# Kernel optimization log

Measured on AMD Instinct MI355X. Metric: run time of the kernel, lower is better.

The kernel has to match this reference:

```python
import jax, jax.numpy as jnp
import numpy as np

B, N, C = 4, 1370, 1024
H, DH = 16, C // 16
N_ROPE = 1369  # patch tokens covered by RoPE (prefix=1 CLS token)


def _rotate_half(x):
    x1, x2 = jnp.split(x, 2, axis=-1)
    return jnp.concatenate([-x2, x1], axis=-1)


def _rope_apply(x, sin, cos):
    return x * cos + _rotate_half(x) * sin


def setup_inputs() -> dict:
    key = jax.random.key(0)
    ks = jax.random.split(key, 7)
    return {
        "x": jax.random.normal(ks[0], (B, N, C), dtype=jnp.float32),
        "sin": jax.random.normal(ks[1], (N_ROPE, DH), dtype=jnp.float32),
        "cos": jax.random.normal(ks[2], (N_ROPE, DH), dtype=jnp.float32),
        "w_qkv": jax.random.normal(ks[3], (C, 3 * C), dtype=jnp.float32) * (C ** -0.5),
        "b_qkv": jax.random.normal(ks[4], (3 * C,), dtype=jnp.float32) * 0.02,
        "w_proj": jax.random.normal(ks[5], (C, C), dtype=jnp.float32) * (C ** -0.5),
        "b_proj": jax.random.normal(ks[6], (C,), dtype=jnp.float32) * 0.02,
    }


def reference(x, sin, cos, w_qkv, b_qkv, w_proj, b_proj):
    b, n, c = x.shape
    # QKV projection -> [3, B, H, N, DH]
    qkv = (x @ w_qkv + b_qkv).reshape(b, n, 3, H, DH).transpose(2, 0, 3, 1, 4)
    q, k, v = qkv[0], qkv[1], qkv[2]
    # RoPE on the last N_ROPE tokens (prefix tokens, e.g. CLS, left untouched)
    prefix = n - sin.shape[-2]
    q = jnp.concatenate([q[:, :, :prefix, :], _rope_apply(q[:, :, prefix:, :], sin, cos)], axis=-2)
    k = jnp.concatenate([k[:, :, :prefix, :], _rope_apply(k[:, :, prefix:, :], sin, cos)], axis=-2)
    # Full attention
    scale = 1.0 / jnp.sqrt(jnp.asarray(DH, dtype=x.dtype))
    attn = jnp.einsum('bhqd,bhkd->bhqk', q, k) * scale
    attn = jax.nn.softmax(attn, axis=-1)
    out = jnp.einsum('bhqk,bhkd->bhqd', attn, v)
    out = out.transpose(0, 2, 1, 3).reshape(b, n, c)
    return out @ w_proj + b_proj
```

## Files before the change

### kernel.cpp

```cpp
#include <hip/hip_runtime.h>
#include <hip/hip_bf16.h>

#define B_ 4
#define N_ 1370
#define C_ 1024
#define H_ 16
#define DH_ 64
#define NR_ 1369
#define M_ (B_*N_)
#define VTS_ 1408
#define ALS 64
#define PLS 72

#define QSCALE 0.1803368801111f

typedef _Float16 f16x8  __attribute__((ext_vector_type(8)));
typedef __bf16   bf16x8 __attribute__((ext_vector_type(8)));
typedef float    f32x4  __attribute__((ext_vector_type(4)));

__device__ __forceinline__ f16x8 ld_frag_h(const unsigned short* p) {
    uint4 u = *(const uint4*)p;
    return __builtin_bit_cast(f16x8, u);
}
__device__ __forceinline__ bf16x8 ld_frag_b(const unsigned short* p) {
    uint4 u = *(const uint4*)p;
    return __builtin_bit_cast(bf16x8, u);
}
__device__ __forceinline__ unsigned short f2h(float f) {
    _Float16 h = (_Float16)f;
    return __builtin_bit_cast(unsigned short, h);
}
__device__ __forceinline__ unsigned short f2bf(float f) {
    __hip_bfloat16 h = __float2bfloat16(f);
    return __builtin_bit_cast(unsigned short, h);
}
__device__ __forceinline__ bf16x8 ones_bf() {
    uint4 u = make_uint4(0x3F803F80u, 0x3F803F80u, 0x3F803F80u, 0x3F803F80u);
    return __builtin_bit_cast(bf16x8, u);
}

__device__ __forceinline__ void load_lds16(const unsigned short* g, unsigned short* l) {
    __builtin_amdgcn_global_load_lds(
        (const __attribute__((address_space(1))) unsigned int*)g,
        (__attribute__((address_space(3))) unsigned int*)l,
        16, 0, 0);
}

#define XBLK 5480
#define WQBLK 768
#define WPBLK 256
__global__ __launch_bounds__(256)
void prep_k(const float* __restrict__ x, unsigned short* __restrict__ xo,
            const float* __restrict__ wq, unsigned short* __restrict__ wqt,
            const float* __restrict__ wp, unsigned short* __restrict__ wpt)
{
    __shared__ unsigned short Th[64][68];
    int bid = blockIdx.x;
    if (bid < XBLK) {
        const int i = bid * 256 + threadIdx.x;
        float4 v = ((const float4*)x)[i];
        ushort4 h;
        h.x = f2h(v.x); h.y = f2h(v.y); h.z = f2h(v.z); h.w = f2h(v.w);
        ((ushort4*)xo)[i] = h;
        return;
    }
    bid -= XBLK;
    const float* w; unsigned short* wt; int Ncol, nb;
    if (bid < WQBLK) { w = wq; wt = wqt; Ncol = 3072; nb = 48; }
    else { bid -= WQBLK; w = wp; wt = wpt; Ncol = 1024; nb = 16; }
    const int tid = threadIdx.x, tx = tid & 15, ty = tid >> 4;
    const int n0 = (bid % nb) * 64, k0 = (bid / nb) * 64;
    #pragma unroll
    for (int i = 0; i < 4; ++i) {
        const int k = ty + i * 16;
        float4 v = *(const float4*)&w[(size_t)(k0 + k) * Ncol + n0 + tx * 4];
        Th[k][tx*4+0] = f2h(v.x); Th[k][tx*4+1] = f2h(v.y);
        Th[k][tx*4+2] = f2h(v.z); Th[k][tx*4+3] = f2h(v.w);
    }
    __syncthreads();
    #pragma unroll
    for (int i = 0; i < 4; ++i) {
        const int n = ty + i * 16;
        ushort4 o;
        o.x = Th[tx*4+0][n]; o.y = Th[tx*4+1][n]; o.z = Th[tx*4+2][n]; o.w = Th[tx*4+3][n];
        *(ushort4*)&wt[(size_t)(n0 + n) * 1024 + k0 + tx * 4] = o;
    }
}

__global__ __launch_bounds__(256)
void transpose_v_k(const unsigned short* __restrict__ v, unsigned short* __restrict__ vt) {
    __shared__ unsigned short Th[64][68];
    const int tid = threadIdx.x, tx = tid & 15, ty = tid >> 4;
    const int bh = blockIdx.y, t0 = blockIdx.x * 64;
    const unsigned short* vp = v + (size_t)bh * N_ * DH_;
    unsigned short* vtp = vt + (size_t)bh * DH_ * VTS_;
    #pragma unroll
    for (int i = 0; i < 4; ++i) {
        const int tok = ty + i * 16;
        const int gtok = t0 + tok;
        ushort4 val;
        if (gtok < N_) val = *(const ushort4*)&vp[(size_t)gtok * DH_ + tx * 4];
        else { val.x = 0; val.y = 0; val.z = 0; val.w = 0; }
        Th[tok][tx*4+0] = val.x; Th[tok][tx*4+1] = val.y;
        Th[tok][tx*4+2] = val.z; Th[tok][tx*4+3] = val.w;
    }
    __syncthreads();
    #pragma unroll
    for (int i = 0; i < 4; ++i) {
        const int d = ty + i * 16;
        ushort4 o;
        o.x = Th[tx*4+0][d]; o.y = Th[tx*4+1][d]; o.z = Th[tx*4+2][d]; o.w = Th[tx*4+3][d];
        *(ushort4*)&vtp[(size_t)d * VTS_ + t0 + tx * 4] = o;
    }
}

__global__ __launch_bounds__(512, 4)
void gemm_qkv8(const unsigned short* __restrict__ A, const unsigned short* __restrict__ Bt,
               const float* __restrict__ bias,
               unsigned short* __restrict__ qb, unsigned short* __restrict__ kb,
               unsigned short* __restrict__ vb,
               const float* __restrict__ sinp, const float* __restrict__ cosp)
{
    __shared__ __align__(16) unsigned short A_s[2][192 * 64];
    __shared__ __align__(16) unsigned short B_s[2][128 * 64];

    const int tid = threadIdx.x;
    const int wave = tid >> 6, lane = tid & 63;
    const int quad = lane >> 4, l16 = lane & 15;

    const int id  = blockIdx.x;
    const int lid = (id & 7) * 87 + (id >> 3);
    const int mblk = lid / 24, nblk = lid - mblk * 24;
    const int m0 = mblk * 192, n0 = nblk * 128;

    const int mwave = (wave >> 1) * 48;
    const int nwave = (wave & 1) * 64;

    const int srow = lane >> 3;
    const int gseg = (lane & 7) ^ srow;

    f32x4 acc[3][4] = {};

    auto stage = [&](int kc, int buf) {
        const int kof = kc * 64;
        #pragma unroll
        for (int i = 0; i < 3; ++i) {
            const int rbase = wave * 24 + i * 8;
            int arow = m0 + rbase + srow;
            if (arow > M_ - 1) arow = M_ - 1;
            load_lds16(A + (size_t)arow * 1024 + kof + gseg * 8, &A_s[buf][rbase * 64]);
        }
        #pragma unroll
        for (int i = 0; i < 2; ++i) {
            const int rbase = wave * 16 + i * 8;
            const int brow = n0 + rbase + srow;
            load_lds16(Bt + (size_t)brow * 1024 + kof + gseg * 8, &B_s[buf][rbase * 64]);
        }
    };

    stage(0, 0);

    for (int kc = 0; kc < 16; ++kc) {
        const int cur = kc & 1;
        __syncthreads();
        if (kc + 1 < 16) stage(kc + 1, cur ^ 1);

        #pragma unroll
        for (int kh = 0; kh < 2; ++kh) {
            const int soff = (((kh * 4 + quad) ^ (l16 & 7)) << 3);
            f16x8 a[3], b[4];
            #pragma unroll
            for (int t = 0; t < 3; ++t)
                a[t] = ld_frag_h(&A_s[cur][(mwave + t * 16 + l16) * 64 + soff]);
            #pragma unroll
            for (int t = 0; t < 4; ++t)
                b[t] = ld_frag_h(&B_s[cur][(nwave + t * 16 + l16) * 64 + soff]);
            #pragma unroll
            for (int i = 0; i < 3; ++i)
                #pragma unroll
                for (int j = 0; j < 4; ++j)
                    acc[i][j] = __builtin_amdgcn_mfma_f32_16x16x32_f16(a[i], b[j], acc[i][j], 0, 0, 0);
        }
    }

    const int nbase = n0 + nwave;
    const int part = nbase >> 10;
    const int h = (nbase & 1023) >> 6;
    #pragma unroll
    for (int i = 0; i < 3; ++i) {
        #pragma unroll
        for (int r = 0; r < 4; ++r) {
            const int gm = m0 + mwave + i * 16 + quad * 4 + r;
            if (gm >= M_) continue;
            const int b = gm / N_;
            const int tok = gm - b * N_;

            float val[4];
            #pragma unroll
            for (int j = 0; j < 4; ++j)
                val[j] = acc[i][j][r] + bias[nbase + j * 16 + l16];

            if (part < 2 && tok >= 1) {
                const float* sp = sinp + (size_t)(tok - 1) * DH_;
                const float* cp = cosp + (size_t)(tok - 1) * DH_;
                const float s0 = sp[l16],      s1 = sp[16 + l16];
                const float s2 = sp[32 + l16], s3 = sp[48 + l16];
                const float c0 = cp[l16],      c1 = cp[16 + l16];
                const float c2 = cp[32 + l16], c3 = cp[48 + l16];
                const float n0v = fmaf(val[0], c0, -val[2] * s0);
                const float n1v = fmaf(val[1], c1, -val[3] * s1);
                const float n2v = fmaf(val[2], c2,  val[0] * s2);
                const float n3v = fmaf(val[3], c3,  val[1] * s3);
                val[0] = n0v; val[1] = n1v; val[2] = n2v; val[3] = n3v;
            }

            const int bh = b * H_ + h;
            #pragma unroll
            for (int j = 0; j < 4; ++j) {
                const int d = j * 16 + l16;
                if (part == 0)      qb[((size_t)bh * N_ + tok) * DH_ + d] = f2h(val[j] * QSCALE);
                else if (part == 1) kb[((size_t)bh * N_ + tok) * DH_ + d] = f2h(val[j]);
                else                vb[((size_t)bh * N_ + tok) * DH_ + d] = f2bf(val[j]);
            }
        }
    }
}

__global__ __launch_bounds__(256)
void gemm_proj2(const unsigned short* __restrict__ A, const unsigned short* __restrict__ Bt,
                const float* __restrict__ bias, float* __restrict__ out)
{
    __shared__ __align__(16) unsigned short A_s[2][64 * 64];
    __shared__ __align__(16) unsigned short B_s[2][128 * 64];

    const int tid = threadIdx.x;
    const int wave = tid >> 6, lane = tid & 63;
    const int quad = lane >> 4, l16 = lane & 15;
    const int m0 = blockIdx.y * 64, n0 = blockIdx.x * 128;
    const int mwave = (wave & 1) * 32, nwave = (wave >> 1) * 64;

    const int srow = lane >> 3;
    const int gseg = (lane & 7) ^ srow;

    f32x4 acc[2][4] = {};

    auto stage = [&](int kc, int buf) {
        const int kof = kc * 64;
        #pragma unroll
        for (int i = 0; i < 2; ++i) {
            const int rbase = wave * 16 + i * 8;
            int arow = m0 + rbase + srow;
            if (arow > M_ - 1) arow = M_ - 1;
            load_lds16(A + (size_t)arow * 1024 + kof + gseg * 8, &A_s[buf][rbase * 64]);
        }
        #pragma unroll
        for (int i = 0; i < 4; ++i) {
            const int rbase = wave * 32 + i * 8;
            const int brow = n0 + rbase + srow;
            load_lds16(Bt + (size_t)brow * 1024 + kof + gseg * 8, &B_s[buf][rbase * 64]);
        }
    };

    stage(0, 0);

    for (int kc = 0; kc < 16; ++kc) {
        const int cur = kc & 1;
        __syncthreads();
        if (kc + 1 < 16) stage(kc + 1, cur ^ 1);

        #pragma unroll
        for (int kh = 0; kh < 2; ++kh) {
            const int soff = (((kh * 4 + quad) ^ (l16 & 7)) << 3);
            f16x8 a[2], b[4];
            #pragma unroll
            for (int t = 0; t < 2; ++t)
                a[t] = ld_frag_h(&A_s[cur][(mwave + t * 16 + l16) * 64 + soff]);
            #pragma unroll
            for (int t = 0; t < 4; ++t)
                b[t] = ld_frag_h(&B_s[cur][(nwave + t * 16 + l16) * 64 + soff]);
            #pragma unroll
            for (int i = 0; i < 2; ++i)
                #pragma unroll
                for (int j = 0; j < 4; ++j)
                    acc[i][j] = __builtin_amdgcn_mfma_f32_16x16x32_f16(a[i], b[j], acc[i][j], 0, 0, 0);
        }
    }

    #pragma unroll
    for (int i = 0; i < 2; ++i) {
        #pragma unroll
        for (int r = 0; r < 4; ++r) {
            const int gm = m0 + mwave + i * 16 + quad * 4 + r;
            if (gm >= M_) continue;
            #pragma unroll
            for (int j = 0; j < 4; ++j) {
                const int gn = n0 + nwave + j * 16 + l16;
                out[(size_t)gm * 1024 + gn] = acc[i][j][r] + bias[gn];
            }
        }
    }
}

__global__ __launch_bounds__(512, 6)
void attn_k(const unsigned short* __restrict__ q, const unsigned short* __restrict__ k,
            const unsigned short* __restrict__ vt, unsigned short* __restrict__ out)
{
    __shared__ __align__(16) unsigned short Ks[2][64 * ALS];
    __shared__ __align__(16) unsigned short Vs[2][64 * ALS];
    __shared__ __align__(16) unsigned short Ps[8 * 16 * PLS];

    const int tid  = threadIdx.x;
    const int wave = tid >> 6, lane = tid & 63;
    const int quad = lane >> 4, l16 = lane & 15;
    const int srow = lane >> 3;
    const int gseg = (lane & 7) ^ srow;

    const int id  = blockIdx.x;
    const int lid = (id & 7) * 88 + (id >> 3);
    const int bh  = lid / 11;
    const int q0  = (lid - bh * 11) * 128;

    const unsigned short* qp  = q  + (size_t)bh * N_ * DH_;
    const unsigned short* kp  = k  + (size_t)bh * N_ * DH_;
    const unsigned short* vtp = vt + (size_t)bh * DH_ * VTS_;

    f16x8 qf[2];
    {
        int qrow = q0 + wave * 16 + l16;
        if (qrow > N_ - 1) qrow = N_ - 1;
        qf[0] = ld_frag_h(qp + (size_t)qrow * DH_ + quad * 8);
        qf[1] = ld_frag_h(qp + (size_t)qrow * DH_ + 32 + quad * 8);
    }

    const bf16x8 onesv = ones_bf();
    f32x4 O[4] = {};
    f32x4 L = {};

    unsigned short* Pw = Ps + wave * 16 * PLS;
    const int so0 = ((quad)     ^ (l16 & 7)) << 3;
    const int so1 = ((4 + quad) ^ (l16 & 7)) << 3;

    auto stage = [&](int ch, int buf) {
        const int k0 = ch * 64;
        const int rbase = wave * 8;
        int krow = k0 + rbase + srow;
        if (krow > N_ - 1) krow = N_ - 1;
        load_lds16(kp + (size_t)krow * DH_ + gseg * 8, &Ks[buf][rbase * ALS]);
        load_lds16(vtp + (size_t)(rbase + srow) * VTS_ + k0 + gseg * 8, &Vs[buf][rbase * ALS]);
    };

    stage(0, 0);

    for (int ch = 0; ch < 22; ++ch) {
        const int k0 = ch * 64;
        const int cur = ch & 1;
        __syncthreads();
        if (ch + 1 < 22) stage(ch + 1, 1 - cur);

        f16x8 kf[4][2];
        #pragma unroll
        for (int t = 0; t < 4; ++t) {
            kf[t][0] = ld_frag_h(&Ks[cur][(t * 16 + l16) * ALS + so0]);
            kf[t][1] = ld_frag_h(&Ks[cur][(t * 16 + l16) * ALS + so1]);
        }
        f32x4 S[4];
        #pragma unroll
        for (int t = 0; t < 4; ++t) {
            f32x4 z = {};
            z = __builtin_amdgcn_mfma_f32_16x16x32_f16(qf[0], kf[t][0], z, 0, 0, 0);
            z = __builtin_amdgcn_mfma_f32_16x16x32_f16(qf[1], kf[t][1], z, 0, 0, 0);
            S[t] = z;
        }
        if (k0 + 64 > N_) {
            #pragma unroll
            for (int t = 0; t < 4; ++t) {
                if (k0 + t * 16 + l16 >= N_) {
                    S[t][0] = -1e30f; S[t][1] = -1e30f;
                    S[t][2] = -1e30f; S[t][3] = -1e30f;
                }
            }
        }

        #pragma unroll
        for (int t = 0; t < 4; ++t) {
            #pragma unroll
            for (int r = 0; r < 4; ++r) {
                const float p = __builtin_amdgcn_exp2f(S[t][r]);
                Pw[(quad * 4 + r) * PLS + t * 16 + l16] = f2bf(p);
            }
        }
        __builtin_amdgcn_wave_barrier();

        bf16x8 pf[2];
        pf[0] = ld_frag_b(&Pw[l16 * PLS + quad * 8]);
        pf[1] = ld_frag_b(&Pw[l16 * PLS + 32 + quad * 8]);

        bf16x8 vf[4][2];
        #pragma unroll
        for (int dt = 0; dt < 4; ++dt) {
            vf[dt][0] = ld_frag_b(&Vs[cur][(dt * 16 + l16) * ALS + so0]);
            vf[dt][1] = ld_frag_b(&Vs[cur][(dt * 16 + l16) * ALS + so1]);
        }
        L = __builtin_amdgcn_mfma_f32_16x16x32_bf16(pf[0], onesv, L, 0, 0, 0);
        L = __builtin_amdgcn_mfma_f32_16x16x32_bf16(pf[1], onesv, L, 0, 0, 0);
        #pragma unroll
        for (int dt = 0; dt < 4; ++dt) {
            O[dt] = __builtin_amdgcn_mfma_f32_16x16x32_bf16(pf[0], vf[dt][0], O[dt], 0, 0, 0);
            O[dt] = __builtin_amdgcn_mfma_f32_16x16x32_bf16(pf[1], vf[dt][1], O[dt], 0, 0, 0);
        }
    }

    const int b = bh >> 4, h = bh & 15;
    #pragma unroll
    for (int r = 0; r < 4; ++r) {
        const int qi = q0 + wave * 16 + quad * 4 + r;
        if (qi < N_) {
            const float inv = 1.0f / L[r];
            unsigned short* op = out + ((size_t)(b * N_ + qi)) * C_ + h * DH_ + l16;
            #pragma unroll
            for (int dt = 0; dt < 4; ++dt) op[dt * 16] = f2h(O[dt][r] * inv);
        }
    }
}

extern "C" void kernel_launch(void* const* d_in, const int* in_sizes, int n_in,
                              void* d_out, int out_size, void* d_ws, size_t ws_size,
                              hipStream_t stream) {
    const float* x      = (const float*)d_in[0];
    const float* sinp   = (const float*)d_in[1];
    const float* cosp   = (const float*)d_in[2];
    const float* w_qkv  = (const float*)d_in[3];
    const float* b_qkv  = (const float*)d_in[4];
    const float* w_proj = (const float*)d_in[5];
    const float* b_proj = (const float*)d_in[6];
    float* out = (float*)d_out;

    unsigned short* p = (unsigned short*)d_ws;
    const size_t xsz  = (size_t)M_ * C_;
    const size_t wqsz = (size_t)3 * C_ * C_;
    const size_t wpsz = (size_t)C_ * C_;
    const size_t hsz  = (size_t)B_ * H_ * N_ * DH_;
    const size_t vtsz = (size_t)B_ * H_ * DH_ * VTS_;
    unsigned short* x_h   = p;            p += xsz;
    unsigned short* wq_t  = p;            p += wqsz;
    unsigned short* wp_t  = p;            p += wpsz;
    unsigned short* q     = p;            p += hsz;
    unsigned short* k     = p;            p += hsz;
    unsigned short* vt    = p;            p += vtsz;
    unsigned short* attnb = p;            p += xsz;
    unsigned short* vb    = attnb;

    prep_k<<<dim3(XBLK + WQBLK + WPBLK), 256, 0, stream>>>(
        x, x_h, w_qkv, wq_t, w_proj, wp_t);

    gemm_qkv8<<<dim3(696), 512, 0, stream>>>(
        x_h, wq_t, b_qkv, q, k, vb, sinp, cosp);

    transpose_v_k<<<dim3(VTS_ / 64, B_ * H_), 256, 0, stream>>>(vb, vt);

    attn_k<<<dim3(11 * B_ * H_), 512, 0, stream>>>(q, k, vt, attnb);

    gemm_proj2<<<dim3(C_ / 128, (M_ + 63) / 64), 256, 0, stream>>>(
        attnb, wp_t, b_proj, out);
}
```

Before: 232.4 us.

## Fuse V transpose into QKV GEMM epilogue via LDS staging

Removes the separate transpose_v_k kernel. The QKV GEMM blocks that produce V now stage their bf16 tile in shared memory transposed and write it straight to the padded V^T layout. The zero padding past token N is moved into extra prep_k blocks. This saves one launch plus a round trip of V through global memory. In exchange the V epilogue adds two block barriers and per-element scalar global stores along the token dimension.

```diff
diff --git a/kernel.cpp b/kernel.cpp
--- a/kernel.cpp
+++ b/kernel.cpp
@@ -11,6 +11,7 @@
 #define VTS_ 1408
 #define ALS 64
 #define PLS 72
+#define SVS 200
 
 #define QSCALE 0.1803368801111f
 
@@ -49,10 +50,12 @@
 #define XBLK 5480
 #define WQBLK 768
 #define WPBLK 256
+#define VTBLK 64
 __global__ __launch_bounds__(256)
 void prep_k(const float* __restrict__ x, unsigned short* __restrict__ xo,
             const float* __restrict__ wq, unsigned short* __restrict__ wqt,
-            const float* __restrict__ wp, unsigned short* __restrict__ wpt)
+            const float* __restrict__ wp, unsigned short* __restrict__ wpt,
+            unsigned short* __restrict__ vt)
 {
     __shared__ unsigned short Th[64][68];
     int bid = blockIdx.x;
@@ -65,6 +68,15 @@
         return;
     }
     bid -= XBLK;
+    if (bid >= WQBLK + WPBLK) {
+        const int bh = bid - (WQBLK + WPBLK);
+        unsigned short* base = vt + (size_t)bh * DH_ * VTS_;
+        for (int e = threadIdx.x; e < DH_ * (VTS_ - N_); e += 256) {
+            const int d = e / (VTS_ - N_), t = e - d * (VTS_ - N_);
+            base[(size_t)d * VTS_ + N_ + t] = 0;
+        }
+        return;
+    }
     const float* w; unsigned short* wt; int Ncol, nb;
     if (bid < WQBLK) { w = wq; wt = wqt; Ncol = 3072; nb = 48; }
     else { bid -= WQBLK; w = wp; wt = wpt; Ncol = 1024; nb = 16; }
@@ -87,42 +99,16 @@
     }
 }
 
-__global__ __launch_bounds__(256)
-void transpose_v_k(const unsigned short* __restrict__ v, unsigned short* __restrict__ vt) {
-    __shared__ unsigned short Th[64][68];
-    const int tid = threadIdx.x, tx = tid & 15, ty = tid >> 4;
-    const int bh = blockIdx.y, t0 = blockIdx.x * 64;
-    const unsigned short* vp = v + (size_t)bh * N_ * DH_;
-    unsigned short* vtp = vt + (size_t)bh * DH_ * VTS_;
-    #pragma unroll
-    for (int i = 0; i < 4; ++i) {
-        const int tok = ty + i * 16;
-        const int gtok = t0 + tok;
-        ushort4 val;
-        if (gtok < N_) val = *(const ushort4*)&vp[(size_t)gtok * DH_ + tx * 4];
-        else { val.x = 0; val.y = 0; val.z = 0; val.w = 0; }
-        Th[tok][tx*4+0] = val.x; Th[tok][tx*4+1] = val.y;
-        Th[tok][tx*4+2] = val.z; Th[tok][tx*4+3] = val.w;
-    }
-    __syncthreads();
-    #pragma unroll
-    for (int i = 0; i < 4; ++i) {
-        const int d = ty + i * 16;
-        ushort4 o;
-        o.x = Th[tx*4+0][d]; o.y = Th[tx*4+1][d]; o.z = Th[tx*4+2][d]; o.w = Th[tx*4+3][d];
-        *(ushort4*)&vtp[(size_t)d * VTS_ + t0 + tx * 4] = o;
-    }
-}
-
 __global__ __launch_bounds__(512, 4)
 void gemm_qkv8(const unsigned short* __restrict__ A, const unsigned short* __restrict__ Bt,
                const float* __restrict__ bias,
                unsigned short* __restrict__ qb, unsigned short* __restrict__ kb,
-               unsigned short* __restrict__ vb,
+               unsigned short* __restrict__ vt,
                const float* __restrict__ sinp, const float* __restrict__ cosp)
 {
-    __shared__ __align__(16) unsigned short A_s[2][192 * 64];
-    __shared__ __align__(16) unsigned short B_s[2][128 * 64];
+    __shared__ __align__(16) unsigned short SMEM[40960];
+    unsigned short* const A_s = SMEM;
+    unsigned short* const B_s = SMEM + 24576;
 
     const int tid = threadIdx.x;
     const int wave = tid >> 6, lane = tid & 63;
@@ -148,13 +134,15 @@
             const int rbase = wave * 24 + i * 8;
             int arow = m0 + rbase + srow;
             if (arow > M_ - 1) arow = M_ - 1;
-            load_lds16(A + (size_t)arow * 1024 + kof + gseg * 8, &A_s[buf][rbase * 64]);
+            load_lds16(A + (size_t)arow * 1024 + kof + gseg * 8,
+                       A_s + buf * 12288 + rbase * 64);
         }
         #pragma unroll
         for (int i = 0; i < 2; ++i) {
             const int rbase = wave * 16 + i * 8;
             const int brow = n0 + rbase + srow;
-            load_lds16(Bt + (size_t)brow * 1024 + kof + gseg * 8, &B_s[buf][rbase * 64]);
+            load_lds16(Bt + (size_t)brow * 1024 + kof + gseg * 8,
+                       B_s + buf * 8192 + rbase * 64);
         }
     };
 
@@ -171,10 +159,10 @@
             f16x8 a[3], b[4];
             #pragma unroll
             for (int t = 0; t < 3; ++t)
-                a[t] = ld_frag_h(&A_s[cur][(mwave + t * 16 + l16) * 64 + soff]);
+                a[t] = ld_frag_h(A_s + cur * 12288 + (mwave + t * 16 + l16) * 64 + soff);
             #pragma unroll
             for (int t = 0; t < 4; ++t)
-                b[t] = ld_frag_h(&B_s[cur][(nwave + t * 16 + l16) * 64 + soff]);
+                b[t] = ld_frag_h(B_s + cur * 8192 + (nwave + t * 16 + l16) * 64 + soff);
             #pragma unroll
             for (int i = 0; i < 3; ++i)
                 #pragma unroll
@@ -184,6 +172,44 @@
     }
 
     const int nbase = n0 + nwave;
+
+    if (n0 >= 2048) {
+        unsigned short* const Sv = SMEM;
+        __syncthreads();
+        #pragma unroll
+        for (int i = 0; i < 3; ++i) {
+            #pragma unroll
+            for (int r = 0; r < 4; ++r) {
+                const int tl = mwave + i * 16 + quad * 4 + r;
+                #pragma unroll
+                for (int j = 0; j < 4; ++j) {
+                    const int c = nwave + j * 16 + l16;
+                    Sv[c * SVS + tl] = f2bf(acc[i][j][r] + bias[nbase + j * 16 + l16]);
+                }
+            }
+        }
+        __syncthreads();
+        const int b0 = m0 / N_;
+        const int cross = (b0 + 1) * N_ - m0;
+        const int hbase = n0 & 1023;
+        for (int cr = 0; cr < 16; ++cr) {
+            const int c = wave * 16 + cr;
+            const int h = (hbase + c) >> 6;
+            const int d = c & 63;
+            #pragma unroll
+            for (int it = 0; it < 3; ++it) {
+                const int tl = it * 64 + lane;
+                const int gm = m0 + tl;
+                if (gm < M_) {
+                    const int b = b0 + (tl >= cross ? 1 : 0);
+                    const int tok = gm - b * N_;
+                    vt[((size_t)((b * H_ + h) * DH_ + d)) * VTS_ + tok] = Sv[c * SVS + tl];
+                }
+            }
+        }
+        return;
+    }
+
     const int part = nbase >> 10;
     const int h = (nbase & 1023) >> 6;
     #pragma unroll
@@ -200,7 +226,7 @@
             for (int j = 0; j < 4; ++j)
                 val[j] = acc[i][j][r] + bias[nbase + j * 16 + l16];
 
-            if (part < 2 && tok >= 1) {
+            if (tok >= 1) {
                 const float* sp = sinp + (size_t)(tok - 1) * DH_;
                 const float* cp = cosp + (size_t)(tok - 1) * DH_;
                 const float s0 = sp[l16],      s1 = sp[16 + l16];
@@ -218,9 +244,8 @@
             #pragma unroll
             for (int j = 0; j < 4; ++j) {
                 const int d = j * 16 + l16;
-                if (part == 0)      qb[((size_t)bh * N_ + tok) * DH_ + d] = f2h(val[j] * QSCALE);
-                else if (part == 1) kb[((size_t)bh * N_ + tok) * DH_ + d] = f2h(val[j]);
-                else                vb[((size_t)bh * N_ + tok) * DH_ + d] = f2bf(val[j]);
+                if (part == 0) qb[((size_t)bh * N_ + tok) * DH_ + d] = f2h(val[j] * QSCALE);
+                else           kb[((size_t)bh * N_ + tok) * DH_ + d] = f2h(val[j]);
             }
         }
     }
@@ -448,15 +473,12 @@
     unsigned short* k     = p;            p += hsz;
     unsigned short* vt    = p;            p += vtsz;
     unsigned short* attnb = p;            p += xsz;
-    unsigned short* vb    = attnb;
-
-    prep_k<<<dim3(XBLK + WQBLK + WPBLK), 256, 0, stream>>>(
-        x, x_h, w_qkv, wq_t, w_proj, wp_t);
+
+    prep_k<<<dim3(XBLK + WQBLK + WPBLK + VTBLK), 256, 0, stream>>>(
+        x, x_h, w_qkv, wq_t, w_proj, wp_t, vt);
 
     gemm_qkv8<<<dim3(696), 512, 0, stream>>>(
-        x_h, wq_t, b_qkv, q, k, vb, sinp, cosp);
-
-    transpose_v_k<<<dim3(VTS_ / 64, B_ * H_), 256, 0, stream>>>(vb, vt);
+        x_h, wq_t, b_qkv, q, k, vt, sinp, cosp);
 
     attn_k<<<dim3(11 * B_ * H_), 512, 0, stream>>>(q, k, vt, attnb);
 
```

Result: faster. 226.1 us, median of 3 (-2.7%).
